# Optimization experiments

Measured on AMD Instinct MI355X. Metric: run time of the kernel, lower is better.

## Reference

```python
import jax, jax.numpy as jnp
import numpy as np

N, F, E = 100000, 128, 1600000


def setup_inputs() -> dict:
    key = jax.random.key(0)
    ks = jax.random.split(key, 10)
    s = 1.0 / np.sqrt(F)
    return {
        "x": jax.random.normal(ks[0], (N, F), jnp.float32),
        "edge_index": jax.random.randint(ks[1], (2, E), 0, N),
        "edge_weight": jax.random.uniform(ks[2], (E,), jnp.float32),
        # EvolveGCNO initial weight (1, F, F) -> squeezed to (F, F)
        "initial_weight": jax.random.normal(ks[3], (F, F), jnp.float32) * s,
        # torch.nn.GRU(F, F) params, gate order (r, z, n)
        "gru_w_ih": jax.random.uniform(ks[4], (3 * F, F), jnp.float32, -s, s),
        "gru_w_hh": jax.random.uniform(ks[5], (3 * F, F), jnp.float32, -s, s),
        "gru_b_ih": jax.random.uniform(ks[6], (3 * F,), jnp.float32, -s, s),
        "gru_b_hh": jax.random.uniform(ks[7], (3 * F,), jnp.float32, -s, s),
        # Linear(F, 1)
        "lin_w": jax.random.uniform(ks[8], (1, F), jnp.float32, -s, s),
        "lin_b": jax.random.uniform(ks[9], (1,), jnp.float32, -s, s),
    }


def _evolve_weight(W0, w_ih, w_hh, b_ih, b_hh):
    # One GRU step: input = W0 rows (batch=F), hidden = W0 rows (first call of EvolveGCNO)
    gi = W0 @ w_ih.T + b_ih  # (F, 3F)
    gh = W0 @ w_hh.T + b_hh
    i_r, i_z, i_n = jnp.split(gi, 3, axis=-1)
    h_r, h_z, h_n = jnp.split(gh, 3, axis=-1)
    r = jax.nn.sigmoid(i_r + h_r)
    z = jax.nn.sigmoid(i_z + h_z)
    n = jnp.tanh(i_n + r * h_n)
    return (1.0 - z) * n + z * W0  # (F, F)


def reference(x, edge_index, edge_weight, initial_weight, gru_w_ih, gru_w_hh,
              gru_b_ih, gru_b_hh, lin_w, lin_b):
    W = _evolve_weight(initial_weight, gru_w_ih, gru_w_hh, gru_b_ih, gru_b_hh)
    n_nodes = x.shape[0]
    row, col = edge_index[0], edge_index[1]  # source, target
    # gcn_norm: add self loops (weight 1), sym-normalize D^-1/2 (A+I) D^-1/2
    loop = jnp.arange(n_nodes)
    row = jnp.concatenate([row, loop])
    col = jnp.concatenate([col, loop])
    w = jnp.concatenate([edge_weight, jnp.ones((n_nodes,), x.dtype)])
    deg = jax.ops.segment_sum(w, col, num_segments=n_nodes)
    dinv = jnp.where(deg > 0, jax.lax.rsqrt(deg), 0.0)
    norm = dinv[row] * w * dinv[col]  # (E+N,)
    xw = x @ W  # (N, F)
    # gather at sources, weighted scatter-add at targets
    h = jax.ops.segment_sum(norm[:, None] * xw[row], col, num_segments=n_nodes)
    h = jax.nn.relu(h)
    return (h @ lin_w.T + lin_b)[:, 0]  # (N,)
```

## Files before the change

kernel.cpp:

```cpp
#include <hip/hip_runtime.h>

#define F 128
#define DEG_SCALE 16777216.0f
#define DEG_INV   (1.0f / 16777216.0f)
#define BUCK_BITS 7
#define BUCK_COLS 128
#define CAP 2304
#define EPT 8
#define WB_STRIDE 136

typedef _Float16 half8 __attribute__((ext_vector_type(8)));
typedef float f32x4 __attribute__((ext_vector_type(4)));
typedef float f32x2 __attribute__((ext_vector_type(2)));

__global__ __launch_bounds__(256) void init_kernel(
    int* __restrict__ cursor, int NZ, int NBUK,
    const float* __restrict__ W0, const float* __restrict__ wih,
    const float* __restrict__ whh, const float* __restrict__ bih,
    const float* __restrict__ bhh, float* __restrict__ W,
    int* __restrict__ offs, int N, int total) {
  __shared__ float w0row[2][F];
  int b = blockIdx.x;
  if (b < NZ) {
    int i = b * 256 + threadIdx.x;
    if (i < NBUK) cursor[i] = 0;
    if (b == 0 && threadIdx.x == 0) offs[N] = total;
    return;
  }
  int half = threadIdx.x >> 7;
  int j = threadIdx.x & 127;
  int i = (b - NZ) * 2 + half;
  w0row[half][j] = W0[i * F + j];
  __syncthreads();
  float ar = 0, az = 0, an = 0, br = 0, bz = 0, bn = 0;
  const float* wi_r = wih + (size_t)j * F;
  const float* wi_z = wih + (size_t)(j + F) * F;
  const float* wi_n = wih + (size_t)(j + 2 * F) * F;
  const float* wh_r = whh + (size_t)j * F;
  const float* wh_z = whh + (size_t)(j + F) * F;
  const float* wh_n = whh + (size_t)(j + 2 * F) * F;
#pragma unroll 4
  for (int k = 0; k < F; ++k) {
    float a = w0row[half][k];
    ar = fmaf(a, wi_r[k], ar);
    az = fmaf(a, wi_z[k], az);
    an = fmaf(a, wi_n[k], an);
    br = fmaf(a, wh_r[k], br);
    bz = fmaf(a, wh_z[k], bz);
    bn = fmaf(a, wh_n[k], bn);
  }
  float gr = ar + bih[j] + br + bhh[j];
  float gz = az + bih[j + F] + bz + bhh[j + F];
  float r = 1.f / (1.f + expf(-gr));
  float z = 1.f / (1.f + expf(-gz));
  float n = tanhf(an + bih[j + 2 * F] + r * (bn + bhh[j + 2 * F]));
  W[i * F + j] = (1.f - z) * n + z * w0row[half][j];
}

__global__ __launch_bounds__(256) void gemm_bin(
    const float* __restrict__ x, const float* __restrict__ W,
    _Float16* __restrict__ xwh, int N, int NG,
    const int* __restrict__ erow, const int* __restrict__ ecol,
    const float* __restrict__ ew, int* __restrict__ cursor,
    uint2* __restrict__ binned, int E, int NBUK, int NBIN) {
  __shared__ __align__(16) char smem[F * WB_STRIDE * 2];
  int bi = blockIdx.x;
  if (bi % 3 == 2) {
    int bb = bi / 3;
    if (bb >= NBIN) return;
    int* cnt = (int*)smem;
    int* base = cnt + 1024;
    int tid = threadIdx.x;
#pragma unroll
    for (int u = tid; u < 1024; u += 256) cnt[u] = 0;
    __syncthreads();
    int e0 = bb * (256 * EPT) + tid;
    int cc[EPT];
    int lrank[EPT];
#pragma unroll
    for (int k = 0; k < EPT; ++k) {
      int e = e0 + k * 256;
      if (e < E) {
        cc[k] = ecol[e];
        lrank[k] = atomicAdd(&cnt[cc[k] >> BUCK_BITS], 1);
      } else cc[k] = -1;
    }
    __syncthreads();
    for (int u = tid; u < NBUK; u += 256) {
      int cu = cnt[u];
      base[u] = cu ? atomicAdd(&cursor[u], cu) : 0;
    }
    __syncthreads();
#pragma unroll
    for (int k = 0; k < EPT; ++k) {
      if (cc[k] >= 0) {
        int e = e0 + k * 256;
        int bk = cc[k] >> BUCK_BITS;
        int pos = base[bk] + lrank[k];
        if (pos < CAP) {
          unsigned cl = (unsigned)(cc[k] & (BUCK_COLS - 1));
          binned[(size_t)bk * CAP + pos] =
              make_uint2((unsigned)erow[e] | (cl << 17), __float_as_uint(ew[e]));
        }
      }
    }
    return;
  }
  int g = (bi / 3) * 2 + (bi % 3);
  if (g >= NG) return;
  _Float16* Wb = (_Float16*)smem;
  int t = threadIdx.x;
  for (int idx = t; idx < F * F; idx += 256) {
    int k = idx >> 7, n = idx & 127;
    Wb[n * WB_STRIDE + k] = (_Float16)W[idx];
  }
  __syncthreads();

  int lane = t & 63, wave = t >> 6;
  int ln = lane & 15, q = lane >> 4;
  int rowb = g * 64 + wave * 16;
  int i = rowb + ln;
  int iclamp = (i < N) ? i : N - 1;
  const float* xp = x + (size_t)iclamp * F + q * 8;

  half8 a[4];
#pragma unroll
  for (int tt = 0; tt < 4; ++tt) {
    float4 v0 = *(const float4*)(xp + 32 * tt);
    float4 v1 = *(const float4*)(xp + 32 * tt + 4);
    half8 av;
    av[0] = (_Float16)v0.x; av[1] = (_Float16)v0.y;
    av[2] = (_Float16)v0.z; av[3] = (_Float16)v0.w;
    av[4] = (_Float16)v1.x; av[5] = (_Float16)v1.y;
    av[6] = (_Float16)v1.z; av[7] = (_Float16)v1.w;
    a[tt] = av;
  }

  f32x4 acc[8];
#pragma unroll
  for (int nt = 0; nt < 8; ++nt) acc[nt] = (f32x4){0.f, 0.f, 0.f, 0.f};

#pragma unroll
  for (int nt = 0; nt < 8; ++nt) {
#pragma unroll
    for (int tt = 0; tt < 4; ++tt) {
      half8 bfrag = *(const half8*)&Wb[(nt * 16 + ln) * WB_STRIDE + tt * 32 + q * 8];
      acc[nt] = __builtin_amdgcn_mfma_f32_16x16x32_f16(a[tt], bfrag, acc[nt], 0, 0, 0);
    }
  }

#pragma unroll
  for (int nt = 0; nt < 8; ++nt) {
#pragma unroll
    for (int r = 0; r < 4; ++r) {
      int rowi = rowb + q * 4 + r;
      if (rowi < N) xwh[(size_t)rowi * F + nt * 16 + ln] = (_Float16)acc[nt][r];
    }
  }
}

__global__ __launch_bounds__(256) void csr_kernel(
    const uint2* __restrict__ binned, const int* __restrict__ cursor,
    int* __restrict__ offs, float* __restrict__ dinv,
    uint2* __restrict__ pairs, int N, int NBUK) {
  __shared__ unsigned long long acc[BUCK_COLS];
  __shared__ float dinvL[BUCK_COLS];
  __shared__ int wbase[BUCK_COLS];
  __shared__ int sc[BUCK_COLS];
  __shared__ int wsum[4];
  int b = blockIdx.x;
  int tid = threadIdx.x;
  if (tid < BUCK_COLS) acc[tid] = 0ull;
  int partial = 0;
  for (int i = tid; i < b; i += 256) partial += cursor[i];
#pragma unroll
  for (int m = 32; m; m >>= 1) partial += __shfl_xor(partial, m);
  if ((tid & 63) == 0) wsum[tid >> 6] = partial;
  __syncthreads();
  int bstart = b * BUCK_COLS + wsum[0] + wsum[1] + wsum[2] + wsum[3];

  int cnt = cursor[b];
  if (cnt > CAP) cnt = CAP;
  const uint2* src = binned + (size_t)b * CAP;
  for (int i = tid; i < cnt; i += 256) {
    uint2 rec = src[i];
    int cl = rec.x >> 17;
    unsigned fx = (unsigned)(__uint_as_float(rec.y) * DEG_SCALE);
    atomicAdd(&acc[cl], ((unsigned long long)1 << 32) | (unsigned long long)fx);
  }
  __syncthreads();
  int node0 = b * BUCK_COLS;
  int cvt1 = 0;
  if (tid < BUCK_COLS) {
    unsigned long long pk = acc[tid];
    int node = node0 + tid;
    if (node < N) {
      cvt1 = (int)(pk >> 32) + 1;
      float deg = (float)(unsigned)(pk & 0xffffffffull) * DEG_INV;
      float dv = rsqrtf(deg + 1.0f);
      dinvL[tid] = dv;
      dinv[node] = dv;
    }
    sc[tid] = cvt1;
  }
  __syncthreads();
  for (int off = 1; off < BUCK_COLS; off <<= 1) {
    int x = 0;
    if (tid < BUCK_COLS && tid >= off) x = sc[tid - off];
    __syncthreads();
    if (tid < BUCK_COLS) sc[tid] += x;
    __syncthreads();
  }
  if (tid < BUCK_COLS) {
    int node = node0 + tid;
    if (node < N) {
      int abs0 = bstart + sc[tid] - cvt1;
      offs[node] = abs0;
      pairs[abs0] = make_uint2((unsigned)node << 8, __float_as_uint(dinvL[tid]));
      wbase[tid] = abs0 + 1;
    }
  }
  __syncthreads();
  for (int i = tid; i < cnt; i += 256) {
    uint2 rec = src[i];
    int cl = rec.x >> 17;
    unsigned r = rec.x & 0x1ffffu;
    float wp = __uint_as_float(rec.y) * dinvL[cl];
    int pos = atomicAdd(&wbase[cl], 1);
    pairs[pos] = make_uint2(r << 8, __float_as_uint(wp));
  }
}

__global__ __launch_bounds__(256) void gather_out(
    const uint2* __restrict__ pairs, const int* __restrict__ offs,
    const float* __restrict__ dinv, const char* __restrict__ xwb,
    const float* __restrict__ linw, const float* __restrict__ linb,
    float* __restrict__ out, int N) {
  int wave = threadIdx.x >> 6;
  int lane = threadIdx.x & 63;
  int node = blockIdx.x * 4 + wave;
  if (node >= N) return;
  int c = lane & 15;
  int q = lane >> 4;

  const char* xb = xwb + (c << 4);
  f32x2 acc[4];
#pragma unroll
  for (int j = 0; j < 4; ++j) acc[j] = (f32x2){0.f, 0.f};

  int start = offs[node], end = offs[node + 1];
  for (int it = start + q; it < end; it += 16) {
    int i1 = (it + 4 < end) ? it + 4 : it;
    int i2 = (it + 8 < end) ? it + 8 : it;
    int i3 = (it + 12 < end) ? it + 12 : it;
    uint2 p0 = pairs[it];
    uint2 p1 = pairs[i1];
    uint2 p2 = pairs[i2];
    uint2 p3 = pairs[i3];
    float n0 = __uint_as_float(p0.y) * dinv[p0.x >> 8];
    float n1 = (it + 4 < end) ? __uint_as_float(p1.y) * dinv[p1.x >> 8] : 0.f;
    float n2 = (it + 8 < end) ? __uint_as_float(p2.y) * dinv[p2.x >> 8] : 0.f;
    float n3 = (it + 12 < end) ? __uint_as_float(p3.y) * dinv[p3.x >> 8] : 0.f;
    half8 x0 = *(const half8*)(xb + p0.x);
    half8 x1 = *(const half8*)(xb + p1.x);
    half8 x2 = *(const half8*)(xb + p2.x);
    half8 x3 = *(const half8*)(xb + p3.x);
    f32x2 nv0 = {n0, n0}, nv1 = {n1, n1}, nv2 = {n2, n2}, nv3 = {n3, n3};
#pragma unroll
    for (int j = 0; j < 4; ++j) {
      f32x2 v; v[0] = (float)x0[2 * j]; v[1] = (float)x0[2 * j + 1];
      acc[j] += nv0 * v;
    }
#pragma unroll
    for (int j = 0; j < 4; ++j) {
      f32x2 v; v[0] = (float)x1[2 * j]; v[1] = (float)x1[2 * j + 1];
      acc[j] += nv1 * v;
    }
#pragma unroll
    for (int j = 0; j < 4; ++j) {
      f32x2 v; v[0] = (float)x2[2 * j]; v[1] = (float)x2[2 * j + 1];
      acc[j] += nv2 * v;
    }
#pragma unroll
    for (int j = 0; j < 4; ++j) {
      f32x2 v; v[0] = (float)x3[2 * j]; v[1] = (float)x3[2 * j + 1];
      acc[j] += nv3 * v;
    }
  }

  float a8[8];
#pragma unroll
  for (int j = 0; j < 8; ++j) a8[j] = acc[j >> 1][j & 1];
#pragma unroll
  for (int j = 0; j < 8; ++j) {
    a8[j] += __shfl_xor(a8[j], 16);
    a8[j] += __shfl_xor(a8[j], 32);
  }

  const float4* lw4 = (const float4*)linw;
  float4 la = lw4[c * 2];
  float4 lb = lw4[c * 2 + 1];
  float p = fmaxf(a8[0], 0.f) * la.x + fmaxf(a8[1], 0.f) * la.y +
            fmaxf(a8[2], 0.f) * la.z + fmaxf(a8[3], 0.f) * la.w +
            fmaxf(a8[4], 0.f) * lb.x + fmaxf(a8[5], 0.f) * lb.y +
            fmaxf(a8[6], 0.f) * lb.z + fmaxf(a8[7], 0.f) * lb.w;
#pragma unroll
  for (int m = 8; m; m >>= 1) p += __shfl_xor(p, m);

  if (lane == 0) out[node] = p + linb[0];
}

extern "C" void kernel_launch(void* const* d_in, const int* in_sizes, int n_in,
                              void* d_out, int out_size, void* d_ws, size_t ws_size,
                              hipStream_t stream) {
  const float* x    = (const float*)d_in[0];
  const int*   ei   = (const int*)d_in[1];
  const float* ew   = (const float*)d_in[2];
  const float* W0   = (const float*)d_in[3];
  const float* wih  = (const float*)d_in[4];
  const float* whh  = (const float*)d_in[5];
  const float* bih  = (const float*)d_in[6];
  const float* bhh  = (const float*)d_in[7];
  const float* linw = (const float*)d_in[8];
  const float* linb = (const float*)d_in[9];

  int N = in_sizes[0] / F;
  int E = in_sizes[2];
  const int* row = ei;
  const int* col = ei + E;
  int NBUK = (N + BUCK_COLS - 1) / BUCK_COLS;
  int total = E + N;

  char* p = (char*)d_ws;
  auto alloc = [&](size_t bytes) {
    char* q = p;
    p += (bytes + 255) & ~(size_t)255;
    return q;
  };
  float*    W      = (float*)alloc((size_t)F * F * 4);
  int*      cursor = (int*)alloc((size_t)NBUK * 4);
  float*    dinv   = (float*)alloc((size_t)N * 4);
  int*      offs   = (int*)alloc(((size_t)N + 1) * 4);
  uint2*    binned = (uint2*)alloc((size_t)NBUK * CAP * 8);
  uint2*    pairs  = (uint2*)alloc(((size_t)total + 16) * 8);
  _Float16* xwh    = (_Float16*)alloc((size_t)N * F * 2);

  int NZ = (NBUK + 255) / 256;
  init_kernel<<<NZ + 64, 256, 0, stream>>>(cursor, NZ, NBUK, W0, wih, whh, bih, bhh,
                                           W, offs, N, total);

  int NG = (N + 63) / 64;
  int NBIN = (E + 256 * EPT - 1) / (256 * EPT);
  int half_g = (NG + 1) / 2;
  int G3 = NBIN > half_g ? NBIN : half_g;
  gemm_bin<<<3 * G3, 256, 0, stream>>>(x, W, xwh, N, NG, row, col, ew, cursor,
                                       binned, E, NBUK, NBIN);

  csr_kernel<<<NBUK, 256, 0, stream>>>(binned, cursor, offs, dinv, pairs, N, NBUK);

  gather_out<<<(N + 3) / 4, 256, 0, stream>>>(pairs, offs, dinv, (const char*)xwh,
                                              linw, linb, (float*)d_out, N);
}
```

Before: 259.7 us.

## Split CSR build into degree and pair kernels, fold full norm into pairs

The CSR kernel is split into two launches: one computes degrees, dinv and offsets, and a second writes the edge pairs with the complete normalization (source dinv times weight times target dinv). With the full norm stored per edge, the gather kernel no longer does a dependent random dinv lookup for every edge. The cost is an extra kernel launch, a second pass over the binned records, and the random dinv reads moving into the pair-building kernel.

```diff
diff --git a/kernel.cpp b/kernel.cpp
--- a/kernel.cpp
+++ b/kernel.cpp
@@ -71,7 +71,6 @@
     int* cnt = (int*)smem;
     int* base = cnt + 1024;
     int tid = threadIdx.x;
-#pragma unroll
     for (int u = tid; u < 1024; u += 256) cnt[u] = 0;
     __syncthreads();
     int e0 = bb * (256 * EPT) + tid;
@@ -159,13 +158,10 @@
   }
 }
 
-__global__ __launch_bounds__(256) void csr_kernel(
+__global__ __launch_bounds__(256) void csr_deg(
     const uint2* __restrict__ binned, const int* __restrict__ cursor,
-    int* __restrict__ offs, float* __restrict__ dinv,
-    uint2* __restrict__ pairs, int N, int NBUK) {
+    int* __restrict__ offs, float* __restrict__ dinv, int N, int NBUK) {
   __shared__ unsigned long long acc[BUCK_COLS];
-  __shared__ float dinvL[BUCK_COLS];
-  __shared__ int wbase[BUCK_COLS];
   __shared__ int sc[BUCK_COLS];
   __shared__ int wsum[4];
   int b = blockIdx.x;
@@ -198,34 +194,52 @@
       cvt1 = (int)(pk >> 32) + 1;
       float deg = (float)(unsigned)(pk & 0xffffffffull) * DEG_INV;
       float dv = rsqrtf(deg + 1.0f);
-      dinvL[tid] = dv;
       dinv[node] = dv;
     }
     sc[tid] = cvt1;
   }
   __syncthreads();
   for (int off = 1; off < BUCK_COLS; off <<= 1) {
-    int x = 0;
-    if (tid < BUCK_COLS && tid >= off) x = sc[tid - off];
-    __syncthreads();
-    if (tid < BUCK_COLS) sc[tid] += x;
-    __syncthreads();
-  }
+    int xv = 0;
+    if (tid < BUCK_COLS && tid >= off) xv = sc[tid - off];
+    __syncthreads();
+    if (tid < BUCK_COLS) sc[tid] += xv;
+    __syncthreads();
+  }
+  if (tid < BUCK_COLS) {
+    int node = node0 + tid;
+    if (node < N) offs[node] = bstart + sc[tid] - cvt1;
+  }
+}
+
+__global__ __launch_bounds__(256) void csr_pairs(
+    const uint2* __restrict__ binned, const int* __restrict__ cursor,
+    const int* __restrict__ offs, const float* __restrict__ dinv,
+    uint2* __restrict__ pairs, int N, int NBUK) {
+  __shared__ float dinvL[BUCK_COLS];
+  __shared__ int wbase[BUCK_COLS];
+  int b = blockIdx.x;
+  int tid = threadIdx.x;
+  int node0 = b * BUCK_COLS;
   if (tid < BUCK_COLS) {
     int node = node0 + tid;
     if (node < N) {
-      int abs0 = bstart + sc[tid] - cvt1;
-      offs[node] = abs0;
-      pairs[abs0] = make_uint2((unsigned)node << 8, __float_as_uint(dinvL[tid]));
-      wbase[tid] = abs0 + 1;
-    }
-  }
-  __syncthreads();
+      int o = offs[node];
+      float dv = dinv[node];
+      dinvL[tid] = dv;
+      wbase[tid] = o + 1;
+      pairs[o] = make_uint2((unsigned)node << 8, __float_as_uint(dv * dv));
+    }
+  }
+  __syncthreads();
+  int cnt = cursor[b];
+  if (cnt > CAP) cnt = CAP;
+  const uint2* src = binned + (size_t)b * CAP;
   for (int i = tid; i < cnt; i += 256) {
     uint2 rec = src[i];
     int cl = rec.x >> 17;
     unsigned r = rec.x & 0x1ffffu;
-    float wp = __uint_as_float(rec.y) * dinvL[cl];
+    float wp = (__uint_as_float(rec.y) * dinvL[cl]) * dinv[r];
     int pos = atomicAdd(&wbase[cl], 1);
     pairs[pos] = make_uint2(r << 8, __float_as_uint(wp));
   }
@@ -233,9 +247,8 @@
 
 __global__ __launch_bounds__(256) void gather_out(
     const uint2* __restrict__ pairs, const int* __restrict__ offs,
-    const float* __restrict__ dinv, const char* __restrict__ xwb,
-    const float* __restrict__ linw, const float* __restrict__ linb,
-    float* __restrict__ out, int N) {
+    const char* __restrict__ xwb, const float* __restrict__ linw,
+    const float* __restrict__ linb, float* __restrict__ out, int N) {
   int wave = threadIdx.x >> 6;
   int lane = threadIdx.x & 63;
   int node = blockIdx.x * 4 + wave;
@@ -257,10 +270,10 @@
     uint2 p1 = pairs[i1];
     uint2 p2 = pairs[i2];
     uint2 p3 = pairs[i3];
-    float n0 = __uint_as_float(p0.y) * dinv[p0.x >> 8];
-    float n1 = (it + 4 < end) ? __uint_as_float(p1.y) * dinv[p1.x >> 8] : 0.f;
-    float n2 = (it + 8 < end) ? __uint_as_float(p2.y) * dinv[p2.x >> 8] : 0.f;
-    float n3 = (it + 12 < end) ? __uint_as_float(p3.y) * dinv[p3.x >> 8] : 0.f;
+    float n0 = __uint_as_float(p0.y);
+    float n1 = (it + 4 < end) ? __uint_as_float(p1.y) : 0.f;
+    float n2 = (it + 8 < end) ? __uint_as_float(p2.y) : 0.f;
+    float n3 = (it + 12 < end) ? __uint_as_float(p3.y) : 0.f;
     half8 x0 = *(const half8*)(xb + p0.x);
     half8 x1 = *(const half8*)(xb + p1.x);
     half8 x2 = *(const half8*)(xb + p2.x);
@@ -356,8 +369,9 @@
   gemm_bin<<<3 * G3, 256, 0, stream>>>(x, W, xwh, N, NG, row, col, ew, cursor,
                                        binned, E, NBUK, NBIN);
 
-  csr_kernel<<<NBUK, 256, 0, stream>>>(binned, cursor, offs, dinv, pairs, N, NBUK);
-
-  gather_out<<<(N + 3) / 4, 256, 0, stream>>>(pairs, offs, dinv, (const char*)xwh,
+  csr_deg<<<NBUK, 256, 0, stream>>>(binned, cursor, offs, dinv, N, NBUK);
+  csr_pairs<<<NBUK, 256, 0, stream>>>(binned, cursor, offs, dinv, pairs, N, NBUK);
+
+  gather_out<<<(N + 3) / 4, 256, 0, stream>>>(pairs, offs, (const char*)xwh,
                                               linw, linb, (float*)d_out, N);
 }
```

After: 264.1 us. Within noise of the previous version (+1.7%).
